# Kernel optimization log

Hardware: AMD Instinct MI355X
Metric: run time of the kernel (lower is better)

## Reference

```python
import jax, jax.numpy as jnp
import numpy as np
from functools import partial

T, B = 1000, 256
STATE_DIM, ACTION_DIM, REWARD_DIM = 64, 8, 1
EMBED = 64
HIDDEN = 256


def setup_inputs() -> dict:
    key = jax.random.key(0)
    ks = jax.random.split(key, 12)
    g = lambda k, shape, fan_in: jax.random.normal(k, shape, jnp.float32) * np.sqrt(2.0 / fan_in)
    return {
        "states": jax.random.normal(ks[0], (T, B, STATE_DIM), jnp.float32),
        "actions": jax.random.normal(ks[1], (T, B, ACTION_DIM), jnp.float32),
        "rewards": jax.random.normal(ks[2], (T, B, REWARD_DIM), jnp.float32),
        # embedding linears (VarianceScaling(2.0) init, zero bias)
        "Ws": g(ks[3], (STATE_DIM, EMBED), STATE_DIM), "bs": jnp.zeros((EMBED,), jnp.float32),
        "Wa": g(ks[4], (ACTION_DIM, EMBED), ACTION_DIM), "ba": jnp.zeros((EMBED,), jnp.float32),
        "Wr": g(ks[5], (REWARD_DIM, EMBED), REWARD_DIM), "br": jnp.zeros((EMBED,), jnp.float32),
        # hk.GRU params: w_i [in, 3H], w_h [H, 3H], b [3H]
        "wi": g(ks[6], (3 * EMBED, 3 * HIDDEN), 3 * EMBED),
        "wh": g(ks[7], (HIDDEN, 3 * HIDDEN), HIDDEN),
        "bg": jnp.zeros((3 * HIDDEN,), jnp.float32),
    }


def _gru_scan(x_seq, h0, wi, wh, bg):
    # x_seq: [T, B, 3*EMBED]; hk.GRU math: z,r = sigmoid gates; a = tanh candidate
    H = HIDDEN
    wh_zr, wh_a = wh[:, : 2 * H], wh[:, 2 * H :]
    b_zr, b_a = bg[: 2 * H], bg[2 * H :]

    def step(h, gx):  # gx = x @ wi precomputed, [B, 3H]
        zr = jax.nn.sigmoid(gx[:, : 2 * H] + h @ wh_zr + b_zr)
        z, r = zr[:, :H], zr[:, H:]
        a = jnp.tanh(gx[:, 2 * H :] + (r * h) @ wh_a + b_a)
        h_next = (1.0 - z) * h + z * a
        return h_next, h_next

    gx_seq = jnp.einsum("tbd,dh->tbh", x_seq, wi)  # one big matmul over all steps
    _, hs = jax.lax.scan(step, h0, gx_seq)
    return hs  # [T, B, H]


def reference(states, actions, rewards, Ws, bs, Wa, ba, Wr, br, wi, wh, bg):
    se = jax.nn.gelu(states @ Ws + bs)
    ae = jax.nn.gelu(actions @ Wa + ba)
    re = jax.nn.gelu(rewards @ Wr + br)
    x = jnp.concatenate((se, ae, re), axis=-1)  # [T, B, 3*EMBED]
    h0 = jnp.zeros((x.shape[1], HIDDEN), x.dtype)
    return _gru_scan(x, h0, wi, wh, bg)
```

## Files before the change

### kernel.cpp

```cpp
#include <hip/hip_runtime.h>
#include <hip/hip_bf16.h>

#define TT   1000
#define BB   256
#define HID  256
#define GD   768
#define XD   192
#define NROW (TT*BB)

typedef __attribute__((ext_vector_type(8))) _Float16 half8;
typedef __attribute__((ext_vector_type(4))) float    float4_t;
typedef __attribute__((ext_vector_type(2))) unsigned uint2_t;

#define MFMA16(A,B,C) __builtin_amdgcn_mfma_f32_16x16x32_f16((A),(B),(C),0,0,0)

__device__ __forceinline__ void gll16(const void* g, void* l) {
  __builtin_amdgcn_global_load_lds((const __attribute__((address_space(1))) void*)g,
                                   (__attribute__((address_space(3))) void*)l, 16, 0, 0);
}

__device__ __forceinline__ unsigned short f2h(float f) {
  _Float16 h = (_Float16)f;
  union { _Float16 h; unsigned short u; } c; c.h = h; return c.u;
}
__device__ __forceinline__ uint2_t pk4h(float4_t v) {
  union { _Float16 h[4]; uint2_t u; } c;
  c.h[0] = (_Float16)v.x; c.h[1] = (_Float16)v.y;
  c.h[2] = (_Float16)v.z; c.h[3] = (_Float16)v.w;
  return c.u;
}
__device__ __forceinline__ float4_t h4_to_f4(uint2_t v) {
  union { uint2_t u; _Float16 h[4]; } c; c.u = v;
  float4_t f;
  f.x = (float)c.h[0]; f.y = (float)c.h[1];
  f.z = (float)c.h[2]; f.w = (float)c.h[3];
  return f;
}
__device__ __forceinline__ float sigx(float x) {
  return __builtin_amdgcn_rcpf(1.0f + __builtin_amdgcn_exp2f(-1.4426950408889634f * x));
}
__device__ __forceinline__ float tanhx(float x) {
  return 1.0f - 2.0f * __builtin_amdgcn_rcpf(1.0f + __builtin_amdgcn_exp2f(2.8853900817779268f * x));
}
__device__ __forceinline__ float4_t sig4(float4_t v){ float4_t o; o.x=sigx(v.x); o.y=sigx(v.y); o.z=sigx(v.z); o.w=sigx(v.w); return o; }
__device__ __forceinline__ float4_t tanh4(float4_t v){ float4_t o; o.x=tanhx(v.x); o.y=tanhx(v.y); o.z=tanhx(v.z); o.w=tanhx(v.w); return o; }
__device__ __forceinline__ float gelu1(float v){
  float c = v + 0.044715f * v * v * v;
  float e = __builtin_amdgcn_exp2f((0.7978845608028654f * 2.8853900817779268f) * c);
  float th = 1.0f - 2.0f * __builtin_amdgcn_rcpf(1.0f + e);
  return 0.5f * v * (1.0f + th);
}

__global__ void k_prep(const float* __restrict__ wi, const float* __restrict__ wh,
                       unsigned short* __restrict__ wiT, unsigned short* __restrict__ whF)
{
  int tid = blockIdx.x * 256 + threadIdx.x;
  if (tid < GD*XD) {
    int n = tid / XD, k = tid - n*XD;
    wiT[tid] = f2h(wi[(size_t)k*GD + n]);
  }
  int t2 = tid - GD*XD;
  if (t2 >= 0 && t2 < 48*8*64*8) {
    int j = t2 & 7, l = (t2 >> 3) & 63, f = t2 >> 9;
    int mf = f >> 3, kf = f & 7;
    int k = kf*32 + ((l >> 4) << 3) + j;
    int n = (mf << 4) + (l & 15);
    whF[t2] = f2h(wh[(size_t)k*GD + n]);
  }
}

__global__ void k_embed(const float* __restrict__ st, const float* __restrict__ ac,
                        const float* __restrict__ rw,
                        const float* __restrict__ Ws, const float* __restrict__ bs,
                        const float* __restrict__ Wa, const float* __restrict__ ba,
                        const float* __restrict__ Wr, const float* __restrict__ br,
                        unsigned short* __restrict__ x)
{
  int lane = threadIdx.x & 63;
  int wid = blockIdx.x * (blockDim.x >> 6) + (threadIdx.x >> 6);
  int nw  = gridDim.x * (blockDim.x >> 6);
  float wsr[64], war[8];
  #pragma unroll
  for (int k = 0; k < 64; ++k) wsr[k] = Ws[k*64 + lane];
  #pragma unroll
  for (int k = 0; k < 8; ++k) war[k] = Wa[k*64 + lane];
  float wrr = Wr[lane];
  float bsv = bs[lane], bav = ba[lane], brv = br[lane];
  for (int row = wid; row < NROW; row += nw) {
    const float4_t* sp = (const float4_t*)(st + (size_t)row*64);
    float a0 = bsv;
    #pragma unroll
    for (int q = 0; q < 16; ++q) {
      float4_t v = sp[q];
      a0 = fmaf(v.x, wsr[4*q+0], a0);
      a0 = fmaf(v.y, wsr[4*q+1], a0);
      a0 = fmaf(v.z, wsr[4*q+2], a0);
      a0 = fmaf(v.w, wsr[4*q+3], a0);
    }
    const float4_t* ap = (const float4_t*)(ac + (size_t)row*8);
    float a1 = bav;
    #pragma unroll
    for (int q = 0; q < 2; ++q) {
      float4_t v = ap[q];
      a1 = fmaf(v.x, war[4*q+0], a1);
      a1 = fmaf(v.y, war[4*q+1], a1);
      a1 = fmaf(v.z, war[4*q+2], a1);
      a1 = fmaf(v.w, war[4*q+3], a1);
    }
    float a2 = fmaf(rw[row], wrr, brv);
    unsigned short* xr = x + (size_t)row*XD;
    xr[lane]       = f2h(gelu1(a0));
    xr[64 + lane]  = f2h(gelu1(a1));
    xr[128 + lane] = f2h(gelu1(a2));
  }
}

__global__ __launch_bounds__(512, 2) void k_gx(const unsigned short* __restrict__ x,
                                               const unsigned short* __restrict__ wiT,
                                               const float* __restrict__ bg,
                                               unsigned short* __restrict__ gx)
{
  __shared__ half8 Xs[24*64];
  __shared__ half8 As[16*64];
  int lane = threadIdx.x & 63;
  int wv   = threadIdx.x >> 6;
  int b    = lane & 15;
  int g8   = (lane >> 4) << 3;
  int row0 = blockIdx.x * 64;
  #pragma unroll
  for (int i = 0; i < 3; ++i) {
    int c = wv*3 + i, nf = c / 6, kf = c - nf*6;
    gll16(x + (size_t)(row0 + nf*16 + b)*XD + kf*32 + g8, &Xs[c*64]);
  }
  int g4 = g8 >> 1;
  float4_t acc[6][4];
  #pragma unroll
  for (int i = 0; i < 6; ++i) {
    float4_t bgv = *(const float4_t*)(bg + (wv + 8*i)*16 + g4);
    #pragma unroll
    for (int nf = 0; nf < 4; ++nf) acc[i][nf] = bgv;
  }
  half8 xb[4];
  for (int kf = 0; kf < 6; ++kf) {
    #pragma unroll
    for (int p = 0; p < 3; ++p) {
      __syncthreads();
      #pragma unroll
      for (int i2 = 0; i2 < 2; ++i2) {
        int q = wv*2 + i2;
        gll16(wiT + (size_t)((p*16 + q)*16 + b)*XD + kf*32 + g8, &As[q*64]);
      }
      __syncthreads();
      if (p == 0) {
        #pragma unroll
        for (int nf = 0; nf < 4; ++nf) xb[nf] = Xs[(nf*6 + kf)*64 + lane];
      }
      half8 af0 = As[wv*64 + lane];
      half8 af1 = As[(wv+8)*64 + lane];
      #pragma unroll
      for (int nf = 0; nf < 4; ++nf) {
        acc[2*p  ][nf] = MFMA16(af0, xb[nf], acc[2*p  ][nf]);
        acc[2*p+1][nf] = MFMA16(af1, xb[nf], acc[2*p+1][nf]);
      }
    }
  }
  #pragma unroll
  for (int i = 0; i < 6; ++i) {
    #pragma unroll
    for (int nf = 0; nf < 4; ++nf) {
      size_t idx = (size_t)(row0 + nf*16 + b)*GD + (wv + 8*i)*16 + g4;
      *(uint2_t*)(gx + idx) = pk4h(acc[i][nf]);
    }
  }
}

__global__ __launch_bounds__(512, 2) void k_gru(const unsigned short* __restrict__ gx,
                                                const unsigned short* __restrict__ whF,
                                                float* __restrict__ out)
{
  extern __shared__ char smem[];
  char* h_lds  = smem;
  char* rh_lds = smem + 8192;
  char* gxb    = smem + 16384;
  const int tid  = threadIdx.x;
  const int lane = tid & 63;
  const int wv   = tid >> 6;
  const int wg   = blockIdx.x;
  const int b    = lane & 15;
  const int g    = lane >> 4;
  const int kr4  = g << 2;
  const int xm   = (b & 7) << 4;

  half8 wz0[8], wz1[8], wr0[8], wr1[8], wa0[8], wa1[8];
  #pragma unroll
  for (int kf = 0; kf < 8; ++kf) {
    wz0[kf] = *(const half8*)(whF + ((size_t)((( 2*wv    )*8 + kf)*64 + lane) << 3));
    wz1[kf] = *(const half8*)(whF + ((size_t)((( 2*wv + 1)*8 + kf)*64 + lane) << 3));
    wr0[kf] = *(const half8*)(whF + ((size_t)(((16 + 2*wv)*8 + kf)*64 + lane) << 3));
    wr1[kf] = *(const half8*)(whF + ((size_t)(((17 + 2*wv)*8 + kf)*64 + lane) << 3));
    wa0[kf] = *(const half8*)(whF + ((size_t)(((32 + 2*wv)*8 + kf)*64 + lane) << 3));
    wa1[kf] = *(const half8*)(whF + ((size_t)(((33 + 2*wv)*8 + kf)*64 + lane) << 3));
  }
  for (int i = tid; i < 2048; i += 512) ((unsigned*)h_lds)[i] = 0u;

  int soff[3], dch[3];
  #pragma unroll
  for (int i = 0; i < 3; ++i) {
    int c = wv*3 + i;
    int doff = c*1024 + lane*16;
    int brow = doff / 1536;
    int cb = doff - brow*1536;
    soff[i] = brow*1536 + (cb ^ ((brow & 7) << 4));
    dch[i] = c*1024;
  }
  const char* gxc = (const char*)gx;
  #pragma unroll
  for (int i = 0; i < 3; ++i)
    gll16(gxc + (size_t)wg*24576 + soff[i], gxb + dch[i]);
  __syncthreads();

  float4_t hf0 = {0.f, 0.f, 0.f, 0.f}, hf1 = hf0;
  const char* hb_base = h_lds + b*512;
  const char* rb_base = rh_lds + b*512;
  const int off_z0 = ((wv*32      + kr4) << 1) ^ xm;
  const int off_z1 = ((wv*32 + 16 + kr4) << 1) ^ xm;

  for (int t = 0; t < TT; ++t) {
    __builtin_amdgcn_sched_barrier(0);
    asm volatile("s_waitcnt vmcnt(2) lgkmcnt(0)" ::: "memory");
    __builtin_amdgcn_s_barrier();
    __builtin_amdgcn_sched_barrier(0);
    if (t + 1 < TT) {
      const char* slab = gxc + (size_t)(t+1)*393216 + (size_t)wg*24576;
      char* dstb = gxb + 24576*((t+1) & 1);
      #pragma unroll
      for (int i = 0; i < 3; ++i) gll16(slab + soff[i], dstb + dch[i]);
    }
    const char* cur = gxb + 24576*(t & 1) + b*1536;
    float4_t az0 = h4_to_f4(*(const uint2_t*)(cur + off_z0));
    float4_t az1 = h4_to_f4(*(const uint2_t*)(cur + off_z1));
    float4_t ar0 = h4_to_f4(*(const uint2_t*)(cur + off_z0 + 512));
    float4_t ar1 = h4_to_f4(*(const uint2_t*)(cur + off_z1 + 512));
    #pragma unroll
    for (int kf = 0; kf < 8; ++kf) {
      half8 hb = *(const half8*)(hb_base + ((kf*64 + (g << 4)) ^ xm));
      az0 = MFMA16(wz0[kf], hb, az0);
      az1 = MFMA16(wz1[kf], hb, az1);
      ar0 = MFMA16(wr0[kf], hb, ar0);
      ar1 = MFMA16(wr1[kf], hb, ar1);
    }
    float4_t z0 = sig4(az0), z1 = sig4(az1);
    float4_t rh0 = sig4(ar0) * hf0, rh1 = sig4(ar1) * hf1;
    *(uint2_t*)(rh_lds + b*512 + off_z0) = pk4h(rh0);
    *(uint2_t*)(rh_lds + b*512 + off_z1) = pk4h(rh1);
    __builtin_amdgcn_sched_barrier(0);
    asm volatile("s_waitcnt lgkmcnt(0)" ::: "memory");
    __builtin_amdgcn_s_barrier();
    __builtin_amdgcn_sched_barrier(0);
    float4_t aa0 = h4_to_f4(*(const uint2_t*)(cur + off_z0 + 1024));
    float4_t aa1 = h4_to_f4(*(const uint2_t*)(cur + off_z1 + 1024));
    #pragma unroll
    for (int kf = 0; kf < 8; ++kf) {
      half8 rb = *(const half8*)(rb_base + ((kf*64 + (g << 4)) ^ xm));
      aa0 = MFMA16(wa0[kf], rb, aa0);
      aa1 = MFMA16(wa1[kf], rb, aa1);
    }
    float4_t a0 = tanh4(aa0), a1 = tanh4(aa1);
    float4_t hn0 = hf0 + z0 * (a0 - hf0);
    float4_t hn1 = hf1 + z1 * (a1 - hf1);
    hf0 = hn0; hf1 = hn1;
    *(uint2_t*)(h_lds + b*512 + off_z0) = pk4h(hn0);
    *(uint2_t*)(h_lds + b*512 + off_z1) = pk4h(hn1);
    float* op = out + (((size_t)t*BB + wg*16 + b) << 8) + wv*32 + kr4;
    *(float4_t*)op = hn0;
    *(float4_t*)(op + 16) = hn1;
  }
}

extern "C" void kernel_launch(void* const* d_in, const int* in_sizes, int n_in,
                              void* d_out, int out_size, void* d_ws, size_t ws_size,
                              hipStream_t stream) {
  (void)in_sizes; (void)n_in; (void)out_size; (void)ws_size;
  const float* states  = (const float*)d_in[0];
  const float* actions = (const float*)d_in[1];
  const float* rewards = (const float*)d_in[2];
  const float* Ws = (const float*)d_in[3];
  const float* bs = (const float*)d_in[4];
  const float* Wa = (const float*)d_in[5];
  const float* ba = (const float*)d_in[6];
  const float* Wr = (const float*)d_in[7];
  const float* br = (const float*)d_in[8];
  const float* wi = (const float*)d_in[9];
  const float* wh = (const float*)d_in[10];
  const float* bg = (const float*)d_in[11];
  char* wsb = (char*)d_ws;
  unsigned short* gx  = (unsigned short*)(wsb);
  unsigned short* x   = (unsigned short*)(wsb + 393216000LL);
  unsigned short* wiT = (unsigned short*)(wsb + 491520000LL);
  unsigned short* whF = (unsigned short*)(wsb + 491814912LL);
  k_prep <<<1344, 256, 0, stream>>>(wi, wh, wiT, whF);
  k_embed<<<1000, 256, 0, stream>>>(states, actions, rewards, Ws, bs, Wa, ba, Wr, br, x);
  k_gx   <<<4000, 512, 0, stream>>>(x, wiT, bg, gx);
  k_gru  <<<16, 512, 65536, stream>>>(gx, whF, (float*)d_out);
}
```

Baseline: 2.400 ms.

## Split GRU recurrence across 16 waves per block, one hidden tile each

The recurrent GRU kernel now runs 1024 threads (16 waves) per block instead of 512. Each wave owns one 16-column hidden tile rather than two, so each wave holds half the weight registers and issues half the MFMA chain per step. The goal is to shorten the per-step serial critical path by spreading the work over more waves. The cost is barriers across twice as many waves, and the gx slab prefetch becomes uneven (only half the threads issue a second load). Some sched_barrier fences are also replaced with plain memory clobbers.

Result: slower. 2.783 ms (+16.0%).

```diff
diff --git a/kernel.cpp b/kernel.cpp
--- a/kernel.cpp
+++ b/kernel.cpp
@@ -174,9 +174,10 @@
   }
 }
 
-__global__ __launch_bounds__(512, 2) void k_gru(const unsigned short* __restrict__ gx,
-                                                const unsigned short* __restrict__ whF,
-                                                float* __restrict__ out)
+__global__ __launch_bounds__(1024, 4)
+void k_gru(const unsigned short* __restrict__ gx,
+           const unsigned short* __restrict__ whF,
+           float* __restrict__ out)
 {
   extern __shared__ char smem[];
   char* h_lds  = smem;
@@ -191,89 +192,75 @@
   const int kr4  = g << 2;
   const int xm   = (b & 7) << 4;
 
-  half8 wz0[8], wz1[8], wr0[8], wr1[8], wa0[8], wa1[8];
+  half8 wz[8], wr[8], wa[8];
   #pragma unroll
   for (int kf = 0; kf < 8; ++kf) {
-    wz0[kf] = *(const half8*)(whF + ((size_t)((( 2*wv    )*8 + kf)*64 + lane) << 3));
-    wz1[kf] = *(const half8*)(whF + ((size_t)((( 2*wv + 1)*8 + kf)*64 + lane) << 3));
-    wr0[kf] = *(const half8*)(whF + ((size_t)(((16 + 2*wv)*8 + kf)*64 + lane) << 3));
-    wr1[kf] = *(const half8*)(whF + ((size_t)(((17 + 2*wv)*8 + kf)*64 + lane) << 3));
-    wa0[kf] = *(const half8*)(whF + ((size_t)(((32 + 2*wv)*8 + kf)*64 + lane) << 3));
-    wa1[kf] = *(const half8*)(whF + ((size_t)(((33 + 2*wv)*8 + kf)*64 + lane) << 3));
-  }
-  for (int i = tid; i < 2048; i += 512) ((unsigned*)h_lds)[i] = 0u;
-
-  int soff[3], dch[3];
-  #pragma unroll
-  for (int i = 0; i < 3; ++i) {
-    int c = wv*3 + i;
-    int doff = c*1024 + lane*16;
-    int brow = doff / 1536;
-    int cb = doff - brow*1536;
-    soff[i] = brow*1536 + (cb ^ ((brow & 7) << 4));
-    dch[i] = c*1024;
-  }
+    wz[kf] = *(const half8*)(whF + ((size_t)(((     wv)*8 + kf)*64 + lane) << 3));
+    wr[kf] = *(const half8*)(whF + ((size_t)(((16 + wv)*8 + kf)*64 + lane) << 3));
+    wa[kf] = *(const half8*)(whF + ((size_t)(((32 + wv)*8 + kf)*64 + lane) << 3));
+  }
+  for (int i = tid; i < 2048; i += 1024) ((unsigned*)h_lds)[i] = 0u;
+
+  const int doff0 = tid << 4;
+  const int brow0 = doff0 / 1536;
+  const int cb0   = doff0 - brow0*1536;
+  const int soff0 = brow0*1536 + (cb0 ^ ((brow0 & 7) << 4));
+  const int doff1 = (1024 + tid) << 4;
+  const int brow1 = doff1 / 1536;
+  const int cb1   = doff1 - brow1*1536;
+  const int soff1 = brow1*1536 + (cb1 ^ ((brow1 & 7) << 4));
+  const bool two  = (tid < 512);
+
   const char* gxc = (const char*)gx;
-  #pragma unroll
-  for (int i = 0; i < 3; ++i)
-    gll16(gxc + (size_t)wg*24576 + soff[i], gxb + dch[i]);
+  {
+    const char* slab0 = gxc + (size_t)wg*24576;
+    gll16(slab0 + soff0, gxb + doff0);
+    if (two) gll16(slab0 + soff1, gxb + doff1);
+  }
   __syncthreads();
 
-  float4_t hf0 = {0.f, 0.f, 0.f, 0.f}, hf1 = hf0;
+  float4_t hf = {0.f, 0.f, 0.f, 0.f};
   const char* hb_base = h_lds + b*512;
   const char* rb_base = rh_lds + b*512;
-  const int off_z0 = ((wv*32      + kr4) << 1) ^ xm;
-  const int off_z1 = ((wv*32 + 16 + kr4) << 1) ^ xm;
+  const int off_z = ((wv*16 + kr4) << 1) ^ xm;
 
   for (int t = 0; t < TT; ++t) {
-    __builtin_amdgcn_sched_barrier(0);
-    asm volatile("s_waitcnt vmcnt(2) lgkmcnt(0)" ::: "memory");
+    asm volatile("s_waitcnt vmcnt(1) lgkmcnt(0)" ::: "memory");
     __builtin_amdgcn_s_barrier();
-    __builtin_amdgcn_sched_barrier(0);
+    asm volatile("" ::: "memory");
     if (t + 1 < TT) {
       const char* slab = gxc + (size_t)(t+1)*393216 + (size_t)wg*24576;
       char* dstb = gxb + 24576*((t+1) & 1);
-      #pragma unroll
-      for (int i = 0; i < 3; ++i) gll16(slab + soff[i], dstb + dch[i]);
+      gll16(slab + soff0, dstb + doff0);
+      if (two) gll16(slab + soff1, dstb + doff1);
     }
     const char* cur = gxb + 24576*(t & 1) + b*1536;
-    float4_t az0 = h4_to_f4(*(const uint2_t*)(cur + off_z0));
-    float4_t az1 = h4_to_f4(*(const uint2_t*)(cur + off_z1));
-    float4_t ar0 = h4_to_f4(*(const uint2_t*)(cur + off_z0 + 512));
-    float4_t ar1 = h4_to_f4(*(const uint2_t*)(cur + off_z1 + 512));
+    float4_t az = h4_to_f4(*(const uint2_t*)(cur + off_z));
+    float4_t ar = h4_to_f4(*(const uint2_t*)(cur + off_z + 512));
     #pragma unroll
     for (int kf = 0; kf < 8; ++kf) {
       half8 hb = *(const half8*)(hb_base + ((kf*64 + (g << 4)) ^ xm));
-      az0 = MFMA16(wz0[kf], hb, az0);
-      az1 = MFMA16(wz1[kf], hb, az1);
-      ar0 = MFMA16(wr0[kf], hb, ar0);
-      ar1 = MFMA16(wr1[kf], hb, ar1);
-    }
-    float4_t z0 = sig4(az0), z1 = sig4(az1);
-    float4_t rh0 = sig4(ar0) * hf0, rh1 = sig4(ar1) * hf1;
-    *(uint2_t*)(rh_lds + b*512 + off_z0) = pk4h(rh0);
-    *(uint2_t*)(rh_lds + b*512 + off_z1) = pk4h(rh1);
-    __builtin_amdgcn_sched_barrier(0);
+      az = MFMA16(wz[kf], hb, az);
+      ar = MFMA16(wr[kf], hb, ar);
+    }
+    float4_t z  = sig4(az);
+    float4_t rh = sig4(ar) * hf;
+    *(uint2_t*)(rh_lds + b*512 + off_z) = pk4h(rh);
     asm volatile("s_waitcnt lgkmcnt(0)" ::: "memory");
     __builtin_amdgcn_s_barrier();
-    __builtin_amdgcn_sched_barrier(0);
-    float4_t aa0 = h4_to_f4(*(const uint2_t*)(cur + off_z0 + 1024));
-    float4_t aa1 = h4_to_f4(*(const uint2_t*)(cur + off_z1 + 1024));
+    asm volatile("" ::: "memory");
+    float4_t aa = h4_to_f4(*(const uint2_t*)(cur + off_z + 1024));
     #pragma unroll
     for (int kf = 0; kf < 8; ++kf) {
       half8 rb = *(const half8*)(rb_base + ((kf*64 + (g << 4)) ^ xm));
-      aa0 = MFMA16(wa0[kf], rb, aa0);
-      aa1 = MFMA16(wa1[kf], rb, aa1);
-    }
-    float4_t a0 = tanh4(aa0), a1 = tanh4(aa1);
-    float4_t hn0 = hf0 + z0 * (a0 - hf0);
-    float4_t hn1 = hf1 + z1 * (a1 - hf1);
-    hf0 = hn0; hf1 = hn1;
-    *(uint2_t*)(h_lds + b*512 + off_z0) = pk4h(hn0);
-    *(uint2_t*)(h_lds + b*512 + off_z1) = pk4h(hn1);
-    float* op = out + (((size_t)t*BB + wg*16 + b) << 8) + wv*32 + kr4;
-    *(float4_t*)op = hn0;
-    *(float4_t*)(op + 16) = hn1;
+      aa = MFMA16(wa[kf], rb, aa);
+    }
+    float4_t a  = tanh4(aa);
+    float4_t hn = hf + z * (a - hf);
+    hf = hn;
+    *(uint2_t*)(h_lds + b*512 + off_z) = pk4h(hn);
+    float* op = out + (((size_t)t*BB + wg*16 + b) << 8) + wv*16 + kr4;
+    *(float4_t*)op = hn;
   }
 }
 
@@ -301,5 +288,5 @@
   k_prep <<<1344, 256, 0, stream>>>(wi, wh, wiT, whF);
   k_embed<<<1000, 256, 0, stream>>>(states, actions, rewards, Ws, bs, Wa, ba, Wr, br, x);
   k_gx   <<<4000, 512, 0, stream>>>(x, wiT, bg, gx);
-  k_gru  <<<16, 512, 65536, stream>>>(gx, whF, (float*)d_out);
-}
+  k_gru  <<<16, 1024, 65536, stream>>>(gx, whF, (float*)d_out);
+}
```
